# Performance work log

Hardware: AMD Instinct MI355X
Metric: run time of the kernel (lower is better)

## Reference

```python
import jax, jax.numpy as jnp
import numpy as np

B, LQ, DIM, NH, NPTS, NL = 8, 9216, 384, 6, 4, 1
HD = DIM // NH            # 64 per head
H0, W0 = 96, 96           # single-level feature map, LKV = 9216
LN_EPS = 1e-5

def layer_norm(x, w, b):
    mu = jnp.mean(x, -1, keepdims=True)
    var = jnp.var(x, -1, keepdims=True)
    return (x - mu) * jax.lax.rsqrt(var + LN_EPS) * w + b

def ms_deform_attn_core(value, spatial_shapes_np, loc, attw):
    # value: [B, LKV, NH, HD]; loc: [B, LQ, NH, NL, NPTS, 2] normalized in [0,1]
    # attw:  [B, LQ, NH, NL, NPTS] (softmaxed over NL*NPTS)
    Bv, _, nH, d = value.shape
    Lq = loc.shape[1]
    per_level = []
    start = 0
    for lvl, (H, W) in enumerate(spatial_shapes_np):
        H, W = int(H), int(W)
        v = jnp.transpose(value[:, start:start + H * W], (0, 2, 1, 3))  # [B,NH,HW,HD]
        start += H * W
        ploc = loc[:, :, :, lvl]                      # [B,LQ,NH,NPTS,2]
        # grid_sample(mode=bilinear, padding=zeros, align_corners=False) pixel coords
        x = ploc[..., 0] * W - 0.5
        y = ploc[..., 1] * H - 0.5
        x0 = jnp.floor(x)
        y0 = jnp.floor(y)
        acc = jnp.zeros((Bv, nH, Lq * NPTS, d), value.dtype)
        for dx in (0.0, 1.0):
            for dy in (0.0, 1.0):
                xi = x0 + dx
                yi = y0 + dy
                w_bil = (1.0 - jnp.abs(x - xi)) * (1.0 - jnp.abs(y - yi))
                valid = (xi >= 0) & (xi < W) & (yi >= 0) & (yi < H)
                idx = (jnp.clip(yi, 0, H - 1) * W + jnp.clip(xi, 0, W - 1)).astype(jnp.int32)
                idx = jnp.transpose(idx, (0, 2, 1, 3)).reshape(Bv, nH, Lq * NPTS)
                g = jnp.take_along_axis(v, idx[..., None], axis=2)  # [B,NH,LQ*NPTS,HD]
                wv = jnp.transpose(w_bil * valid, (0, 2, 1, 3)).reshape(Bv, nH, Lq * NPTS, 1)
                acc = acc + g * wv
        per_level.append(acc.reshape(Bv, nH, Lq, NPTS, d))
    samp = jnp.stack(per_level, axis=3)               # [B,NH,LQ,NL,NPTS,HD]
    aw = jnp.transpose(attw, (0, 2, 1, 3, 4))         # [B,NH,LQ,NL,NPTS]
    out = jnp.einsum('bhqlpd,bhqlp->bqhd', samp, aw)
    return out.reshape(Bv, Lq, nH * d)

def _forward(query, reference_points, feat, spatial_shapes_np,
             qn_w, qn_b, fn_w, fn_b, w_value, b_value, w_off, b_off,
             w_attn, b_attn, w_out, b_out, gamma):
    q = layer_norm(query, qn_w, qn_b)
    f = layer_norm(feat, fn_w, fn_b)
    value = (f @ w_value + b_value).reshape(B, -1, NH, HD)
    off = (q @ w_off + b_off).reshape(B, LQ, NH, NL, NPTS, 2)
    attw = jax.nn.softmax((q @ w_attn + b_attn).reshape(B, LQ, NH, NL * NPTS), -1)
    attw = attw.reshape(B, LQ, NH, NL, NPTS)
    # offset_normalizer = (W, H) per level
    norm = jnp.asarray(np.ascontiguousarray(spatial_shapes_np[:, ::-1]), jnp.float32)
    loc = reference_points[:, :, None, :, None, :] + off / norm[None, None, None, :, None, :]
    attn_out = ms_deform_attn_core(value, spatial_shapes_np, loc, attw)
    attn_out = attn_out @ w_out + b_out
    return query + gamma * attn_out

def setup_inputs():
    key = jax.random.key(0)
    ks = jax.random.split(key, 16)
    s = 0.02
    return {
        "query": jax.random.normal(ks[0], (B, LQ, DIM), jnp.float32),
        "reference_points": jax.random.uniform(ks[1], (B, LQ, NL, 2), dtype=jnp.float32),
        "feat": jax.random.normal(ks[2], (B, H0 * W0, DIM), jnp.float32),
        "spatial_shapes": jnp.array([[H0, W0]], jnp.int32),
        "level_start_index": jnp.array([0], jnp.int32),
        "qn_w": jnp.ones((DIM,), jnp.float32),
        "qn_b": jnp.zeros((DIM,), jnp.float32),
        "fn_w": jnp.ones((DIM,), jnp.float32),
        "fn_b": jnp.zeros((DIM,), jnp.float32),
        "w_value": s * jax.random.normal(ks[3], (DIM, DIM), jnp.float32),
        "b_value": jnp.zeros((DIM,), jnp.float32),
        "w_off": s * jax.random.normal(ks[4], (DIM, NH * NL * NPTS * 2), jnp.float32),
        "b_off": 0.5 * jax.random.normal(ks[5], (NH * NL * NPTS * 2,), jnp.float32),
        "w_attn": s * jax.random.normal(ks[6], (DIM, NH * NL * NPTS), jnp.float32),
        "b_attn": jnp.zeros((NH * NL * NPTS,), jnp.float32),
        "w_out": s * jax.random.normal(ks[7], (DIM, DIM), jnp.float32),
        "b_out": jnp.zeros((DIM,), jnp.float32),
        "gamma": 0.1 * jax.random.normal(ks[8], (DIM,), jnp.float32),
    }

def reference(query, reference_points, feat, spatial_shapes, level_start_index,
              qn_w, qn_b, fn_w, fn_b, w_value, b_value, w_off, b_off,
              w_attn, b_attn, w_out, b_out, gamma):
    ss = np.asarray(spatial_shapes)
    return _forward(query, reference_points, feat, ss,
                    qn_w, qn_b, fn_w, fn_b, w_value, b_value, w_off, b_off,
                    w_attn, b_attn, w_out, b_out, gamma)
```

## Files before the change

### kernel.cpp

```cpp
#include <hip/hip_runtime.h>
#include <hip/hip_bf16.h>
#include <math.h>

#define Bsz   8
#define LQ    9216
#define DIM   384
#define NH    6
#define NPTS  4
#define HD    64
#define H0    96
#define W0    96
#define NROWS (Bsz * LQ)
#define LN_EPS 1e-5f

typedef __attribute__((ext_vector_type(8))) short short8;
typedef __attribute__((ext_vector_type(4))) float f32x4;

__device__ __forceinline__ void load_lds16(const void* g, void* l) {
    __builtin_amdgcn_global_load_lds(
        (const __attribute__((address_space(1))) void*)g,
        (__attribute__((address_space(3))) void*)l,
        16, 0, 0);
}

__device__ __forceinline__ float bf_lo(unsigned u) { return __uint_as_float(u << 16); }
__device__ __forceinline__ float bf_hi(unsigned u) { return __uint_as_float(u & 0xffff0000u); }

__global__ __launch_bounds__(256) void lnorm_kernel(
    const float* __restrict__ X,
    const float* __restrict__ w, const float* __restrict__ bvec,
    __hip_bfloat16* __restrict__ Y)
{
    int wave = threadIdx.x >> 6, lane = threadIdx.x & 63;
    int row = blockIdx.x * 4 + wave;
    const float* x = X + (size_t)row * DIM;
    float2 v[3];
    float s = 0.f, sq = 0.f;
#pragma unroll
    for (int i = 0; i < 3; ++i) {
        v[i] = *(const float2*)&x[lane * 2 + i * 128];
        s  += v[i].x + v[i].y;
        sq += v[i].x * v[i].x + v[i].y * v[i].y;
    }
#pragma unroll
    for (int off = 1; off < 64; off <<= 1) {
        s  += __shfl_xor(s,  off, 64);
        sq += __shfl_xor(sq, off, 64);
    }
    float mu   = s * (1.f / DIM);
    float rstd = rsqrtf(sq * (1.f / DIM) - mu * mu + LN_EPS);
#pragma unroll
    for (int i = 0; i < 3; ++i) {
        int p = lane * 2 + i * 128;
        float2 ww = *(const float2*)&w[p];
        float2 bb = *(const float2*)&bvec[p];
        __hip_bfloat162 o;
        o.x = __float2bfloat16((v[i].x - mu) * rstd * ww.x + bb.x);
        o.y = __float2bfloat16((v[i].y - mu) * rstd * ww.y + bb.y);
        *(__hip_bfloat162*)&Y[(size_t)row * DIM + p] = o;
    }
}

__global__ __launch_bounds__(256) void wtrans_kernel(
    const float* __restrict__ wv, const float* __restrict__ wo,
    const float* __restrict__ woff, const float* __restrict__ watt,
    __hip_bfloat16* __restrict__ WtV, __hip_bfloat16* __restrict__ WtO,
    __hip_bfloat16* __restrict__ WtS)
{
    int gid = blockIdx.x * 256 + threadIdx.x;
    if (gid < 147456) {
        int n = gid / 384, k = gid % 384;
        WtV[gid] = __float2bfloat16(wv[k * 384 + n]);
    } else if (gid < 294912) {
        int i = gid - 147456;
        int n = i / 384, k = i % 384;
        WtO[i] = __float2bfloat16(wo[k * 384 + n]);
    } else {
        int i = gid - 294912;
        int n = i / 384, k = i % 384;
        float v = 0.f;
        if (n < 48)      v = woff[k * 48 + n];
        else if (n < 72) v = watt[k * 24 + (n - 48)];
        WtS[i] = __float2bfloat16(v);
    }
}

template<int MODE>
__global__ __launch_bounds__(256) void gemm16_kernel(
    const __hip_bfloat16* __restrict__ A,
    const __hip_bfloat16* __restrict__ Bt,
    const float* __restrict__ bias,
    const float* __restrict__ bias2,
    const float* __restrict__ resid,
    const float* __restrict__ gamma,
    void* __restrict__ out0,
    void* __restrict__ out1)
{
    __shared__ short As[128 * 32];
    __shared__ short Bs[128 * 32];

    const int t    = threadIdx.x;
    const int lane = t & 63;
    const int w    = t >> 6;
    const int wm   = w >> 1, wn = w & 1;
    const int row0 = blockIdx.y * 128;
    const int col0 = blockIdx.x * 128;
    const int lm   = lane & 15, lq = lane >> 4;

    f32x4 acc[4][4];
#pragma unroll
    for (int i = 0; i < 4; ++i)
#pragma unroll
        for (int j = 0; j < 4; ++j)
            acc[i][j] = (f32x4){0.f, 0.f, 0.f, 0.f};

    for (int k0 = 0; k0 < 384; k0 += 32) {
#pragma unroll
        for (int j = 0; j < 2; ++j) {
            int seg = w * 2 + j;
            int rr  = seg * 16 + (lane >> 2);
            const char* gA = (const char*)(A  + ((size_t)(row0 + rr) * 384 + k0)) + (lane & 3) * 16;
            const char* gB = (const char*)(Bt + ((size_t)(col0 + rr) * 384 + k0)) + (lane & 3) * 16;
            load_lds16(gA, (char*)As + seg * 1024);
            load_lds16(gB, (char*)Bs + seg * 1024);
        }
        __syncthreads();

        short8 af[4], bf[4];
#pragma unroll
        for (int i = 0; i < 4; ++i) {
            af[i] = *(const short8*)&As[(wm * 64 + i * 16 + lm) * 32 + lq * 8];
            bf[i] = *(const short8*)&Bs[(wn * 64 + i * 16 + lm) * 32 + lq * 8];
        }
#pragma unroll
        for (int i = 0; i < 4; ++i)
#pragma unroll
            for (int j = 0; j < 4; ++j)
                acc[i][j] = __builtin_amdgcn_mfma_f32_16x16x32_bf16(af[i], bf[j], acc[i][j], 0, 0, 0);
        __syncthreads();
    }

#pragma unroll
    for (int i = 0; i < 4; ++i) {
#pragma unroll
        for (int j = 0; j < 4; ++j) {
            const int col = col0 + wn * 64 + j * 16 + lm;
#pragma unroll
            for (int r = 0; r < 4; ++r) {
                const int row = row0 + wm * 64 + i * 16 + lq * 4 + r;
                float v = acc[i][j][r];
                if (MODE == 0) {
                    v += bias[col];
                    int b = row / LQ, pix = row - b * LQ;
                    int h = col >> 6, d = col & 63;
                    ((__hip_bfloat16*)out0)[(((size_t)(b * NH + h)) * LQ + pix) * 64 + d] =
                        __float2bfloat16(v);
                } else if (MODE == 1) {
                    v += bias[col];
                    size_t o = (size_t)row * 384 + col;
                    ((float*)out0)[o] = resid[o] + gamma[col] * v;
                } else {
                    if (col < 48)
                        ((float*)out0)[(size_t)row * 48 + col] = v + bias[col];
                    else if (col < 72)
                        ((float*)out1)[(size_t)row * 24 + (col - 48)] = v + bias2[col - 48];
                }
            }
        }
    }
}

__global__ __launch_bounds__(256) void locsoftmax_kernel(
    const float* __restrict__ offbuf, const float* __restrict__ attbuf,
    const float* __restrict__ refpts, float4* __restrict__ smp)
{
    int gid = blockIdx.x * blockDim.x + threadIdx.x;
    int row = gid / NH;
    int h   = gid % NH;
    int b   = row / LQ, q = row - b * LQ;
    size_t task = (size_t)(b * NH + h) * LQ + q;

    const float rx = refpts[row * 2 + 0];
    const float ry = refpts[row * 2 + 1];

    const float* off = offbuf + (size_t)row * (NH * NPTS * 2) + h * (NPTS * 2);
    const float* att = attbuf + (size_t)row * (NH * NPTS)     + h * NPTS;

    float l0 = att[0], l1 = att[1], l2 = att[2], l3 = att[3];
    float m  = fmaxf(fmaxf(l0, l1), fmaxf(l2, l3));
    float e[4] = {expf(l0 - m), expf(l1 - m), expf(l2 - m), expf(l3 - m)};
    float inv = 1.f / (e[0] + e[1] + e[2] + e[3]);

#pragma unroll
    for (int p = 0; p < NPTS; ++p) {
        float x = (rx + off[p * 2 + 0] * (1.f / W0)) * (float)W0 - 0.5f;
        float y = (ry + off[p * 2 + 1] * (1.f / H0)) * (float)H0 - 0.5f;
        smp[task * 4 + p] = make_float4(x, y, e[p] * inv, 0.f);
    }
}

__global__ __launch_bounds__(256) void sample_kernel(
    const __hip_bfloat16* __restrict__ vt,
    const float4* __restrict__ smp,
    __hip_bfloat16* __restrict__ out)
{
    const int wave = threadIdx.x >> 6, lane = threadIdx.x & 63;
    const int slot = lane >> 4;
    const int c4   = lane & 15;
    const int task = (blockIdx.x * 4 + wave) * 4 + slot;
    const int bh   = task / LQ;
    const int q    = task - bh * LQ;
    const int b    = bh / NH, h = bh - b * NH;

    const __hip_bfloat16* vbase = vt + (size_t)bh * LQ * 64;

    float a0 = 0.f, a1 = 0.f, a2 = 0.f, a3 = 0.f;

#pragma unroll
    for (int p = 0; p < NPTS; ++p) {
        float4 s = smp[(size_t)task * 4 + p];
        float x = s.x, y = s.y, wgt = s.z;
        float xf = floorf(x), yf = floorf(y);
        int   x0 = (int)xf,   y0 = (int)yf;
        float fx = x - xf,    fy = y - yf;
        float gx0 = 1.f - fx, gx1 = fx;
        float gy0w = (1.f - fy) * wgt, gy1w = fy * wgt;

#pragma unroll
        for (int cy = 0; cy < 2; ++cy) {
            const int   yi = y0 + cy;
            const float wy = cy ? gy1w : gy0w;
            const bool  vy = (unsigned)yi < H0;
            const int   yc = min(max(yi, 0), H0 - 1);
#pragma unroll
            for (int cx = 0; cx < 2; ++cx) {
                const int xi = x0 + cx;
                float wc = wy * (cx ? gx1 : gx0);
                if (!vy || (unsigned)xi >= W0) wc = 0.f;
                const int xc = min(max(xi, 0), W0 - 1);
                const uint2 raw = *(const uint2*)(vbase + (size_t)(yc * W0 + xc) * 64 + c4 * 4);
                a0 = fmaf(wc, bf_lo(raw.x), a0);
                a1 = fmaf(wc, bf_hi(raw.x), a1);
                a2 = fmaf(wc, bf_lo(raw.y), a2);
                a3 = fmaf(wc, bf_hi(raw.y), a3);
            }
        }
    }

    const int row = b * LQ + q;
    __hip_bfloat162 o01, o23;
    o01.x = __float2bfloat16(a0); o01.y = __float2bfloat16(a1);
    o23.x = __float2bfloat16(a2); o23.y = __float2bfloat16(a3);
    __hip_bfloat162* op = (__hip_bfloat162*)(out + (size_t)row * DIM + h * HD + c4 * 4);
    op[0] = o01;
    op[1] = o23;
}

extern "C" void kernel_launch(void* const* d_in, const int* in_sizes, int n_in,
                              void* d_out, int out_size, void* d_ws, size_t ws_size,
                              hipStream_t stream)
{
    const float* query   = (const float*)d_in[0];
    const float* refpts  = (const float*)d_in[1];
    const float* feat    = (const float*)d_in[2];
    const float* qn_w    = (const float*)d_in[5];
    const float* qn_b    = (const float*)d_in[6];
    const float* fn_w    = (const float*)d_in[7];
    const float* fn_b    = (const float*)d_in[8];
    const float* w_value = (const float*)d_in[9];
    const float* b_value = (const float*)d_in[10];
    const float* w_off   = (const float*)d_in[11];
    const float* b_off   = (const float*)d_in[12];
    const float* w_attn  = (const float*)d_in[13];
    const float* b_attn  = (const float*)d_in[14];
    const float* w_out   = (const float*)d_in[15];
    const float* b_out   = (const float*)d_in[16];
    const float* gamma   = (const float*)d_in[17];

    char* wsb = (char*)d_ws;
    __hip_bfloat16* Q16    = (__hip_bfloat16*)wsb;
    __hip_bfloat16* F16    = (__hip_bfloat16*)(wsb + 56623104);
    __hip_bfloat16* vtrans = (__hip_bfloat16*)(wsb + 113246208);
    __hip_bfloat16* att16  = (__hip_bfloat16*)(wsb + 169869312);
    float*          offbuf = (float*)(wsb + 226492416);
    float*          attbuf = (float*)(wsb + 240648192);
    __hip_bfloat16* WtV    = (__hip_bfloat16*)(wsb + 247726080);
    __hip_bfloat16* WtO    = (__hip_bfloat16*)(wsb + 248020992);
    __hip_bfloat16* WtS    = (__hip_bfloat16*)(wsb + 248315904);
    float4*         smp    = (float4*)wsb;
    float* outp = (float*)d_out;

    lnorm_kernel<<<NROWS / 4, 256, 0, stream>>>(query, qn_w, qn_b, Q16);
    lnorm_kernel<<<NROWS / 4, 256, 0, stream>>>(feat,  fn_w, fn_b, F16);

    wtrans_kernel<<<1344, 256, 0, stream>>>(w_value, w_out, w_off, w_attn,
                                            WtV, WtO, WtS);

    gemm16_kernel<0><<<dim3(3, NROWS / 128), 256, 0, stream>>>(
        F16, WtV, b_value, nullptr, nullptr, nullptr, vtrans, nullptr);

    gemm16_kernel<2><<<dim3(1, NROWS / 128), 256, 0, stream>>>(
        Q16, WtS, b_off, b_attn, nullptr, nullptr, offbuf, attbuf);

    locsoftmax_kernel<<<(NROWS * NH) / 256, 256, 0, stream>>>(
        offbuf, attbuf, refpts, smp);

    sample_kernel<<<(NROWS * NH) / 16, 256, 0, stream>>>(
        vtrans, smp, att16);

    gemm16_kernel<1><<<dim3(3, NROWS / 128), 256, 0, stream>>>(
        att16, WtO, b_out, nullptr, query, gamma, outp, nullptr);
}
```

Measured before the change: 534.8 us.

## Double-buffer LDS tiles in bf16 GEMM to overlap global loads with MFMA

The GEMM kernel now keeps two LDS buffers for the A and B tiles. It issues the async global-to-LDS load for the next K slice before computing on the current one, and needs one barrier per iteration instead of two. The goal is to hide global load latency behind the MFMA work. LDS usage doubles to 32KB per block, which may lower occupancy.

```diff
diff --git a/kernel.cpp b/kernel.cpp
--- a/kernel.cpp
+++ b/kernel.cpp
@@ -96,8 +96,8 @@
     void* __restrict__ out0,
     void* __restrict__ out1)
 {
-    __shared__ short As[128 * 32];
-    __shared__ short Bs[128 * 32];
+    __shared__ short As[2][128 * 32];
+    __shared__ short Bs[2][128 * 32];
 
     const int t    = threadIdx.x;
     const int lane = t & 63;
@@ -107,6 +107,22 @@
     const int col0 = blockIdx.x * 128;
     const int lm   = lane & 15, lq = lane >> 4;
 
+    const int seg0 = w * 2;
+    const int rr0  = seg0 * 16 + (lane >> 2);
+    const int rr1  = rr0 + 16;
+    const size_t boff = (size_t)(lane & 3) * 16;
+
+    auto STAGE = [&](int bf, int k0) {
+        const char* gA0 = (const char*)(A  + ((size_t)(row0 + rr0) * 384 + k0)) + boff;
+        const char* gA1 = (const char*)(A  + ((size_t)(row0 + rr1) * 384 + k0)) + boff;
+        const char* gB0 = (const char*)(Bt + ((size_t)(col0 + rr0) * 384 + k0)) + boff;
+        const char* gB1 = (const char*)(Bt + ((size_t)(col0 + rr1) * 384 + k0)) + boff;
+        load_lds16(gA0, (char*)As[bf] + seg0 * 1024);
+        load_lds16(gA1, (char*)As[bf] + seg0 * 1024 + 1024);
+        load_lds16(gB0, (char*)Bs[bf] + seg0 * 1024);
+        load_lds16(gB1, (char*)Bs[bf] + seg0 * 1024 + 1024);
+    };
+
     f32x4 acc[4][4];
 #pragma unroll
     for (int i = 0; i < 4; ++i)
@@ -114,30 +130,26 @@
         for (int j = 0; j < 4; ++j)
             acc[i][j] = (f32x4){0.f, 0.f, 0.f, 0.f};
 
-    for (int k0 = 0; k0 < 384; k0 += 32) {
-#pragma unroll
-        for (int j = 0; j < 2; ++j) {
-            int seg = w * 2 + j;
-            int rr  = seg * 16 + (lane >> 2);
-            const char* gA = (const char*)(A  + ((size_t)(row0 + rr) * 384 + k0)) + (lane & 3) * 16;
-            const char* gB = (const char*)(Bt + ((size_t)(col0 + rr) * 384 + k0)) + (lane & 3) * 16;
-            load_lds16(gA, (char*)As + seg * 1024);
-            load_lds16(gB, (char*)Bs + seg * 1024);
+    STAGE(0, 0);
+    __syncthreads();
+
+    for (int kt = 0; kt < 12; ++kt) {
+        const int cur = kt & 1;
+        if (kt < 11) STAGE(cur ^ 1, (kt + 1) * 32);
+
+        short8 af[4], bfr[4];
+#pragma unroll
+        for (int i = 0; i < 4; ++i) {
+            af[i]  = *(const short8*)&As[cur][(wm * 64 + i * 16 + lm) * 32 + lq * 8];
+            bfr[i] = *(const short8*)&Bs[cur][(wn * 64 + i * 16 + lm) * 32 + lq * 8];
         }
-        __syncthreads();
-
-        short8 af[4], bf[4];
-#pragma unroll
-        for (int i = 0; i < 4; ++i) {
-            af[i] = *(const short8*)&As[(wm * 64 + i * 16 + lm) * 32 + lq * 8];
-            bf[i] = *(const short8*)&Bs[(wn * 64 + i * 16 + lm) * 32 + lq * 8];
-        }
 #pragma unroll
         for (int i = 0; i < 4; ++i)
 #pragma unroll
             for (int j = 0; j < 4; ++j)
-                acc[i][j] = __builtin_amdgcn_mfma_f32_16x16x32_bf16(af[i], bf[j], acc[i][j], 0, 0, 0);
-        __syncthreads();
+                acc[i][j] = __builtin_amdgcn_mfma_f32_16x16x32_bf16(af[i], bfr[j], acc[i][j], 0, 0, 0);
+
+        if (kt < 11) __syncthreads();
     }
 
 #pragma unroll
```

After: 598.7 us. +11.9%, slower.
